# Performance work log

Measured on AMD Instinct MI355X. Metric: run time of the kernel, lower is better.

## Reference

```python
import jax, jax.numpy as jnp
import numpy as np

N = 100000
E = 1600000
NEG_SLOPE = 0.2

def _gat_layer(x, src, dst, W, a_s, a_d, b, n):
    # GATConv (heads=1): h = xW; alpha_ij = softmax_i(leaky_relu(a_s.h_j + a_d.h_i))
    h = x @ W                                   # [N, F]
    s_src = h @ a_s                             # [N]
    s_dst = h @ a_d                             # [N]
    logits = jax.nn.leaky_relu(s_src[src] + s_dst[dst], NEG_SLOPE)  # [E]
    m = jax.ops.segment_max(logits, dst, num_segments=n)
    m = jnp.where(jnp.isfinite(m), m, 0.0)
    w = jnp.exp(logits - m[dst])
    denom = jax.ops.segment_sum(w, dst, num_segments=n)
    alpha = w / (denom[dst] + 1e-16)            # neighbor softmax per target node
    out = jax.ops.segment_sum(alpha[:, None] * h[src], dst, num_segments=n)
    return out + b

def setup_inputs() -> dict:
    key = jax.random.key(0)
    ks = jax.random.split(key, 12)
    def glorot(k, shape):
        fan = shape[0] + shape[-1] if len(shape) > 1 else shape[0]
        return jax.random.normal(k, shape, jnp.float32) * jnp.sqrt(2.0 / fan)
    x = jax.random.normal(ks[0], (N, 128), jnp.float32)
    edge_index = jax.random.randint(ks[1], (2, E), 0, N, dtype=jnp.int32)
    return {
        'x': x, 'edge_index': edge_index,
        'W1': glorot(ks[2], (128, 64)), 'a1s': glorot(ks[3], (64,)), 'a1d': glorot(ks[4], (64,)), 'b1': jnp.zeros((64,), jnp.float32),
        'W2': glorot(ks[5], (64, 64)), 'a2s': glorot(ks[6], (64,)), 'a2d': glorot(ks[7], (64,)), 'b2': jnp.zeros((64,), jnp.float32),
        'W3': glorot(ks[8], (64, 32)), 'a3s': glorot(ks[9], (32,)), 'a3d': glorot(ks[10], (32,)), 'b3': jnp.zeros((32,), jnp.float32),
    }

def reference(x, edge_index, W1, a1s, a1d, b1, W2, a2s, a2d, b2, W3, a3s, a3d, b3):
    n = x.shape[0]
    # PyG GATConv adds self-loops by default
    loops = jnp.arange(n, dtype=edge_index.dtype)
    src = jnp.concatenate([edge_index[0], loops])
    dst = jnp.concatenate([edge_index[1], loops])
    h = _gat_layer(x, src, dst, W1, a1s, a1d, b1, n)
    h = jax.nn.relu(h)  # dropout is identity in eval mode
    h = _gat_layer(h, src, dst, W2, a2s, a2d, b2, n)
    h = jax.nn.relu(h)
    h = _gat_layer(h, src, dst, W3, a3s, a3d, b3, n)
    return jax.nn.log_softmax(h, axis=1)
```

## Files before the change

kernel.cpp:

```cpp
#include <hip/hip_runtime.h>
#include <hip/hip_fp16.h>
#include <cstddef>
#include <cstdint>

#define NEG_SLOPE 0.2f

__device__ __forceinline__ unsigned short f2bf(float f) {
    unsigned int u = __float_as_uint(f);
    u = (u + 0x7fff + ((u >> 16) & 1)) >> 16;
    return (unsigned short)u;
}
__device__ __forceinline__ float bf_lo(unsigned int u) { return __uint_as_float(u << 16); }
__device__ __forceinline__ float bf_hi(unsigned int u) { return __uint_as_float(u & 0xffff0000u); }

typedef __attribute__((ext_vector_type(8))) short bf16x8;
typedef __attribute__((ext_vector_type(4))) float f32x4;
typedef __attribute__((ext_vector_type(2))) float f32x2;


constexpr int BIN_BLOCKS = 256;
constexpr int MAX_NBK = 1024;

__global__ __launch_bounds__(256) void zero_k(int* __restrict__ p, int n) {
    int i = blockIdx.x * blockDim.x + threadIdx.x;
    if (i < n) p[i] = 0;
}

__global__ __launch_bounds__(256) void bin_hist_k(const int* __restrict__ dst, int E,
                                                  int* __restrict__ btot,
                                                  int* __restrict__ blkoff,
                                                  int nbk, int chunk) {
    __shared__ int hist[MAX_NBK];
    for (int i = threadIdx.x; i < nbk; i += 256) hist[i] = 0;
    __syncthreads();
    const int lo = blockIdx.x * chunk;
    const int hi = min(lo + chunk, E);
    for (int e = lo + threadIdx.x; e < hi; e += 256)
        atomicAdd(&hist[dst[e] >> 7], 1);
    __syncthreads();
    const int B = gridDim.x;
    for (int i = threadIdx.x; i < nbk; i += 256)
        blkoff[i * B + blockIdx.x] = atomicAdd(&btot[i], hist[i]);
}

__global__ __launch_bounds__(256) void scan_small_k(const int* __restrict__ btot,
                                                    int* __restrict__ obk, int nbk) {
    __shared__ int sh[MAX_NBK];
    const int tid = threadIdx.x;
    for (int i = tid; i < nbk; i += 256) sh[i] = btot[i];
    __syncthreads();
    if (tid == 0) {
        int run = 0;
        for (int i = 0; i < nbk; ++i) { int c = sh[i]; sh[i] = run; run += c; }
        obk[nbk] = run;
    }
    __syncthreads();
    for (int i = tid; i < nbk; i += 256) obk[i] = sh[i];
}

__global__ __launch_bounds__(256) void bin_scatter_k(const int* __restrict__ ei, int E,
                                                     const int* __restrict__ obk,
                                                     const int* __restrict__ blkoff,
                                                     int* __restrict__ eb, int nbk,
                                                     int chunk) {
    __shared__ int cur[MAX_NBK];
    __shared__ int off_s[MAX_NBK];
    const int B = gridDim.x;
    for (int i = threadIdx.x; i < nbk; i += 256) {
        cur[i] = 0;
        off_s[i] = obk[i] + blkoff[i * B + blockIdx.x];
    }
    __syncthreads();
    const int lo = blockIdx.x * chunk;
    const int hi = min(lo + chunk, E);
    for (int e = lo + threadIdx.x; e < hi; e += 256) {
        int s = ei[e];
        int d = ei[E + e];
        int b = d >> 7;
        int idx = atomicAdd(&cur[b], 1);
        eb[off_s[b] + idx] = (s << 7) | (d & 127);
    }
}

__global__ __launch_bounds__(256) void bucket_build_k(const int* __restrict__ eb,
                                                      const int* __restrict__ obk,
                                                      int* __restrict__ row_ptr,
                                                      int* __restrict__ col,
                                                      int n, int nbk) {
    __shared__ int c[128];
    __shared__ int rp[128];
    const int b = blockIdx.x;
    const int t = threadIdx.x;
    const int beg = obk[b];
    const int end = obk[b + 1];
    const int bbase = beg + b * 128;
    if (t < 128) c[t] = 1;
    __syncthreads();
    for (int i = beg + t; i < end; i += 256)
        atomicAdd(&c[eb[i] & 127], 1);
    __syncthreads();
    if (t < 64) {
        int v0 = c[2 * t], v1 = c[2 * t + 1];
        int pair = v0 + v1;
        int inc = pair;
        for (int o = 1; o < 64; o <<= 1) {
            int u = __shfl_up(inc, o);
            if (t >= o) inc += u;
        }
        int ex = inc - pair;
        rp[2 * t] = bbase + ex;
        rp[2 * t + 1] = bbase + ex + v0;
    }
    __syncthreads();
    const int node = b * 128 + t;
    if (t < 128 && node < n) {
        row_ptr[node] = rp[t];
        col[rp[t]] = node;
    }
    if (b == 0 && t == 0) row_ptr[n] = obk[nbk] + n;
    __syncthreads();
    if (t < 128) c[t] = 1;
    __syncthreads();
    for (int i = beg + t; i < end; i += 256) {
        int p = eb[i];
        int dl = p & 127;
        int idx = atomicAdd(&c[dl], 1);
        col[rp[dl] + idx] = p >> 7;
    }
}


template <int K, int F, bool BIN>
__launch_bounds__(256)
__global__ void gemm_mfma_k(const void* __restrict__ xin, const float* __restrict__ W,
                            const float* __restrict__ a_s, const float* __restrict__ a_d,
                            unsigned short* __restrict__ hb, float* __restrict__ ss,
                            float* __restrict__ sd, int n) {
    constexpr int MT = 64;
    constexpr int KP = K + 8;
    constexpr int NT = F / 16;
    constexpr int KC = K / 32;

    __shared__ unsigned short xb[MT * KP];
    __shared__ unsigned short wb[F * KP];

    const int tid = threadIdx.x;
    const int lane = tid & 63;
    const int wv = tid >> 6;
    const int base = blockIdx.x * MT;

    if (BIN) {
        const unsigned short* x = (const unsigned short*)xin;
        for (int i = tid; i < MT * K / 8; i += 256) {
            int row = i / (K / 8);
            int c8 = i % (K / 8);
            uint4 v = make_uint4(0u, 0u, 0u, 0u);
            if (base + row < n)
                v = *(const uint4*)&x[(size_t)(base + row) * K + 8 * c8];
            *(uint4*)&xb[row * KP + 8 * c8] = v;
        }
    } else {
        const float* x = (const float*)xin;
        for (int i = tid; i < MT * K / 4; i += 256) {
            int row = i / (K / 4);
            int c4 = i % (K / 4);
            float4 v = make_float4(0.f, 0.f, 0.f, 0.f);
            if (base + row < n)
                v = *(const float4*)&x[(size_t)(base + row) * K + 4 * c4];
            ushort4 b;
            b.x = f2bf(v.x); b.y = f2bf(v.y); b.z = f2bf(v.z); b.w = f2bf(v.w);
            *(ushort4*)&xb[row * KP + 4 * c4] = b;
        }
    }
    for (int i = tid; i < K * F / 4; i += 256) {
        int k = i / (F / 4);
        int n4 = i % (F / 4);
        float4 v = *(const float4*)&W[(size_t)k * F + 4 * n4];
        wb[(4 * n4 + 0) * KP + k] = f2bf(v.x);
        wb[(4 * n4 + 1) * KP + k] = f2bf(v.y);
        wb[(4 * n4 + 2) * KP + k] = f2bf(v.z);
        wb[(4 * n4 + 3) * KP + k] = f2bf(v.w);
    }
    __syncthreads();

    const int mrow = lane & 15;
    const int quad = lane >> 4;

    f32x4 acc[NT];
#pragma unroll
    for (int t = 0; t < NT; ++t) acc[t] = (f32x4){0.f, 0.f, 0.f, 0.f};

#pragma unroll
    for (int kc = 0; kc < KC; ++kc) {
        const int kof = kc * 32 + quad * 8;
        bf16x8 af = *(const bf16x8*)&xb[(wv * 16 + mrow) * KP + kof];
#pragma unroll
        for (int t = 0; t < NT; ++t) {
            bf16x8 bf = *(const bf16x8*)&wb[(t * 16 + mrow) * KP + kof];
            acc[t] = __builtin_amdgcn_mfma_f32_16x16x32_bf16(af, bf, acc[t], 0, 0, 0);
        }
    }

    float as_c[NT], ad_c[NT];
#pragma unroll
    for (int t = 0; t < NT; ++t) { as_c[t] = a_s[t * 16 + mrow]; ad_c[t] = a_d[t * 16 + mrow]; }

#pragma unroll
    for (int r = 0; r < 4; ++r) {
        const int node = base + wv * 16 + quad * 4 + r;
        float ps = 0.f, pd = 0.f;
#pragma unroll
        for (int t = 0; t < NT; ++t) {
            ps = fmaf(acc[t][r], as_c[t], ps);
            pd = fmaf(acc[t][r], ad_c[t], pd);
        }
#pragma unroll
        for (int o = 1; o < 16; o <<= 1) {
            ps += __shfl_xor(ps, o);
            pd += __shfl_xor(pd, o);
        }
        if (node < n) {
#pragma unroll
            for (int t = 0; t < NT; ++t)
                hb[(size_t)node * F + t * 16 + mrow] = f2bf(acc[t][r]);
            if (mrow == 0) { ss[node] = ps; sd[node] = pd; }
        }
    }
}


template <int F, int S, bool RELU, bool LOGSM, bool OUTB>
__launch_bounds__(256)
__global__ void gat_agg_k(const int* __restrict__ row_ptr, const int* __restrict__ col,
                          const unsigned short* __restrict__ hb,
                          const float* __restrict__ ss, const float* __restrict__ sd,
                          const float* __restrict__ bias,
                          void* __restrict__ outv, int n) {
    constexpr int NPW = 64 / S;
    constexpr int NL = F / 8;
    constexpr int Q = S / NL;
    const int lane = threadIdx.x & 63;
    const int ls   = lane % S;
    const int q    = ls / NL;
    const int cl   = ls % NL;
    const int lbase = lane - ls;
    const int wave = (blockIdx.x * blockDim.x + threadIdx.x) >> 6;
    const int node = wave * NPW + lane / S;
    if (node >= n) return;

    const int beg = row_ptr[node];
    const int end = row_ptr[node + 1];
    const float sdv = sd[node];
    float z0 = ss[node] + sdv;
    z0 = (z0 > 0.f) ? z0 : NEG_SLOPE * z0;

    float s = 0.f;
    f32x2 acc2[4];
#pragma unroll
    for (int i = 0; i < 4; ++i) acc2[i] = (f32x2){0.f, 0.f};

    for (int base = beg; base < end; base += S) {
        const int j = base + ls;
        int   c = 0;
        float logit = -__builtin_inff();
        if (j < end) {
            c = col[j];
            float z = ss[c] + sdv;
            logit = (z > 0.f) ? z : NEG_SLOPE * z;
        }
        const float w = __expf(logit - z0);
        s += w;
        const unsigned int pk = ((unsigned int)f2bf(w) << 17) | (unsigned int)c;

        auto gather = [&](int tt) {
            const unsigned int pe = __shfl(pk, lbase + Q * tt + q);
            const int ct = (int)(pe & 0x1ffffu);
            const float wt = __uint_as_float((pe >> 17) << 16);
            const uint4 hv = *(const uint4*)&hb[(size_t)ct * F + 8 * cl];
            f32x2 p;
            p.x = bf_lo(hv.x); p.y = bf_hi(hv.x); acc2[0] += p * wt;
            p.x = bf_lo(hv.y); p.y = bf_hi(hv.y); acc2[1] += p * wt;
            p.x = bf_lo(hv.z); p.y = bf_hi(hv.z); acc2[2] += p * wt;
            p.x = bf_lo(hv.w); p.y = bf_hi(hv.w); acc2[3] += p * wt;
        };

        const int cnt = min(S, end - base);
        int t = 0;
        for (; Q * (t + 3) < cnt; t += 4) {
            gather(t); gather(t + 1); gather(t + 2); gather(t + 3);
        }
        for (; Q * (t + 1) < cnt; t += 2) { gather(t); gather(t + 1); }
        if (Q * t < cnt) gather(t);
    }

#pragma unroll
    for (int o = S / 2; o; o >>= 1) s += __shfl_xor(s, o);
    float val[8] = {acc2[0].x, acc2[0].y, acc2[1].x, acc2[1].y,
                    acc2[2].x, acc2[2].y, acc2[3].x, acc2[3].y};
#pragma unroll
    for (int o = NL; o < S; o <<= 1) {
#pragma unroll
        for (int i = 0; i < 8; ++i) val[i] += __shfl_xor(val[i], o);
    }

    const float inv = 1.f / (s + 1e-16f);
#pragma unroll
    for (int i = 0; i < 8; ++i) {
        val[i] = val[i] * inv + bias[8 * cl + i];
        if (RELU) val[i] = fmaxf(val[i], 0.f);
    }
    if (LOGSM) {
        float lm = val[0];
#pragma unroll
        for (int i = 1; i < 8; ++i) lm = fmaxf(lm, val[i]);
#pragma unroll
        for (int o = 1; o < NL; o <<= 1) lm = fmaxf(lm, __shfl_xor(lm, o));
        float ex = 0.f;
#pragma unroll
        for (int i = 0; i < 8; ++i) ex += __expf(val[i] - lm);
#pragma unroll
        for (int o = 1; o < NL; o <<= 1) ex += __shfl_xor(ex, o);
        const float lse = lm + __logf(ex);
#pragma unroll
        for (int i = 0; i < 8; ++i) val[i] -= lse;
    }
    if (q == 0) {
        if (OUTB) {
            unsigned short* out = (unsigned short*)outv;
            ushort4 p0, p1;
            p0.x = f2bf(val[0]); p0.y = f2bf(val[1]); p0.z = f2bf(val[2]); p0.w = f2bf(val[3]);
            p1.x = f2bf(val[4]); p1.y = f2bf(val[5]); p1.z = f2bf(val[6]); p1.w = f2bf(val[7]);
            *(ushort4*)&out[(size_t)node * F + 8 * cl] = p0;
            *(ushort4*)&out[(size_t)node * F + 8 * cl + 4] = p1;
        } else {
            float* out = (float*)outv;
            float4 v0 = make_float4(val[0], val[1], val[2], val[3]);
            float4 v1 = make_float4(val[4], val[5], val[6], val[7]);
            *(float4*)&out[(size_t)node * F + 8 * cl] = v0;
            *(float4*)&out[(size_t)node * F + 8 * cl + 4] = v1;
        }
    }
}


extern "C" void kernel_launch(void* const* d_in, const int* in_sizes, int n_in,
                              void* d_out, int out_size, void* d_ws, size_t ws_size,
                              hipStream_t stream) {
    const float* x  = (const float*)d_in[0];
    const int*   ei = (const int*)d_in[1];
    const float* W1 = (const float*)d_in[2];
    const float* a1s = (const float*)d_in[3];
    const float* a1d = (const float*)d_in[4];
    const float* b1  = (const float*)d_in[5];
    const float* W2 = (const float*)d_in[6];
    const float* a2s = (const float*)d_in[7];
    const float* a2d = (const float*)d_in[8];
    const float* b2  = (const float*)d_in[9];
    const float* W3 = (const float*)d_in[10];
    const float* a3s = (const float*)d_in[11];
    const float* a3d = (const float*)d_in[12];
    const float* b3  = (const float*)d_in[13];

    const int N = in_sizes[0] / 128;
    const int E = in_sizes[1] / 2;
    const int NBK = (N + 127) / 128;
    const int B = BIN_BLOCKS;

    char* wp = (char*)d_ws;
    auto alloc = [&](size_t bytes) -> void* {
        void* p = wp;
        wp += (bytes + 255) & ~(size_t)255;
        return p;
    };
    int* row_ptr = (int*)alloc((size_t)(N + 1) * 4);
    int* col     = (int*)alloc((size_t)(E + N) * 4);
    unsigned short* hb  = (unsigned short*)alloc((size_t)N * 64 * 2);
    float* ss  = (float*)alloc((size_t)N * 4);
    float* sd  = (float*)alloc((size_t)N * 4);
    unsigned short* o1b = (unsigned short*)alloc((size_t)N * 64 * 2);
    unsigned short* o2b = (unsigned short*)alloc((size_t)N * 64 * 2);
    int* btot   = (int*)alloc((size_t)NBK * 4);
    int* blkoff = (int*)alloc((size_t)NBK * B * 4);
    int* obk    = (int*)alloc((size_t)(NBK + 1) * 4);
    int* eb     = (int*)alloc((size_t)E * 4);

    const int chunk = (E + B - 1) / B;

    zero_k<<<(NBK + 255) / 256, 256, 0, stream>>>(btot, NBK);
    bin_hist_k<<<B, 256, 0, stream>>>(ei + E, E, btot, blkoff, NBK, chunk);
    scan_small_k<<<1, 256, 0, stream>>>(btot, obk, NBK);
    bin_scatter_k<<<B, 256, 0, stream>>>(ei, E, obk, blkoff, eb, NBK, chunk);
    bucket_build_k<<<NBK, 256, 0, stream>>>(eb, obk, row_ptr, col, N, NBK);

    const int GB = (N + 63) / 64;

    gemm_mfma_k<128, 64, false><<<GB, 256, 0, stream>>>(x, W1, a1s, a1d, hb, ss, sd, N);
    gat_agg_k<64, 32, true, false, true><<<(N + 7) / 8, 256, 0, stream>>>(
        row_ptr, col, hb, ss, sd, b1, o1b, N);

    gemm_mfma_k<64, 64, true><<<GB, 256, 0, stream>>>(o1b, W2, a2s, a2d, hb, ss, sd, N);
    gat_agg_k<64, 32, true, false, true><<<(N + 7) / 8, 256, 0, stream>>>(
        row_ptr, col, hb, ss, sd, b2, o2b, N);

    gemm_mfma_k<64, 32, true><<<GB, 256, 0, stream>>>(o2b, W3, a3s, a3d, hb, ss, sd, N);
    gat_agg_k<32, 16, false, true, false><<<(N + 15) / 16, 256, 0, stream>>>(
        row_ptr, col, hb, ss, sd, b3, d_out, N);
}
```

Baseline: 309.0 us.

## Fuse GAT aggregation with next layer's GEMM and parallelize bucket scan

Adds agg_gemm_k, which runs the neighbour-softmax aggregation of layers 1 and 2 into a shared-memory tile and then feeds it straight into the next layer's bf16 MFMA GEMM and attention-score dot products. This drops the round trip of the intermediate activations through global memory and removes two kernel launches. Each layer now gets its own h/ss/sd buffers, and the single-thread prefix scan becomes a wavefront shuffle scan. The aggregation replaces the running max with a self-loop logit shift and packs bf16 weights next to 17-bit column indices, which caps node ids at 131072. Half of the 512 threads sit idle during the GEMM phase.

```diff
diff --git a/kernel.cpp b/kernel.cpp
--- a/kernel.cpp
+++ b/kernel.cpp
@@ -1,5 +1,4 @@
 #include <hip/hip_runtime.h>
-#include <hip/hip_fp16.h>
 #include <cstddef>
 #include <cstdint>
 
@@ -49,10 +48,21 @@
     const int tid = threadIdx.x;
     for (int i = tid; i < nbk; i += 256) sh[i] = btot[i];
     __syncthreads();
-    if (tid == 0) {
+    if (tid < 64) {
         int run = 0;
-        for (int i = 0; i < nbk; ++i) { int c = sh[i]; sh[i] = run; run += c; }
-        obk[nbk] = run;
+        for (int b0 = 0; b0 < nbk; b0 += 64) {
+            const int i = b0 + tid;
+            int v = (i < nbk) ? sh[i] : 0;
+            int inc = v;
+#pragma unroll
+            for (int o = 1; o < 64; o <<= 1) {
+                int u = __shfl_up(inc, o);
+                if (tid >= o) inc += u;
+            }
+            if (i < nbk) sh[i] = run + inc - v;
+            run += __shfl(inc, 63);
+        }
+        if (tid == 0) obk[nbk] = run;
     }
     __syncthreads();
     for (int i = tid; i < nbk; i += 256) obk[i] = sh[i];
@@ -130,9 +140,9 @@
 }
 
 
-template <int K, int F, bool BIN>
+template <int K, int F>
 __launch_bounds__(256)
-__global__ void gemm_mfma_k(const void* __restrict__ xin, const float* __restrict__ W,
+__global__ void gemm_mfma_k(const float* __restrict__ x, const float* __restrict__ W,
                             const float* __restrict__ a_s, const float* __restrict__ a_d,
                             unsigned short* __restrict__ hb, float* __restrict__ ss,
                             float* __restrict__ sd, int n) {
@@ -149,37 +159,25 @@
     const int wv = tid >> 6;
     const int base = blockIdx.x * MT;
 
-    if (BIN) {
-        const unsigned short* x = (const unsigned short*)xin;
-        for (int i = tid; i < MT * K / 8; i += 256) {
-            int row = i / (K / 8);
-            int c8 = i % (K / 8);
-            uint4 v = make_uint4(0u, 0u, 0u, 0u);
-            if (base + row < n)
-                v = *(const uint4*)&x[(size_t)(base + row) * K + 8 * c8];
-            *(uint4*)&xb[row * KP + 8 * c8] = v;
-        }
-    } else {
-        const float* x = (const float*)xin;
-        for (int i = tid; i < MT * K / 4; i += 256) {
-            int row = i / (K / 4);
-            int c4 = i % (K / 4);
-            float4 v = make_float4(0.f, 0.f, 0.f, 0.f);
-            if (base + row < n)
-                v = *(const float4*)&x[(size_t)(base + row) * K + 4 * c4];
-            ushort4 b;
-            b.x = f2bf(v.x); b.y = f2bf(v.y); b.z = f2bf(v.z); b.w = f2bf(v.w);
-            *(ushort4*)&xb[row * KP + 4 * c4] = b;
-        }
+    for (int i = tid; i < MT * K / 4; i += 256) {
+        int row = i / (K / 4);
+        int c4 = i % (K / 4);
+        float4 v = make_float4(0.f, 0.f, 0.f, 0.f);
+        if (base + row < n)
+            v = *(const float4*)&x[(size_t)(base + row) * K + 4 * c4];
+        ushort4 b;
+        b.x = f2bf(v.x); b.y = f2bf(v.y); b.z = f2bf(v.z); b.w = f2bf(v.w);
+        *(ushort4*)&xb[row * KP + 4 * c4] = b;
     }
     for (int i = tid; i < K * F / 4; i += 256) {
-        int k = i / (F / 4);
-        int n4 = i % (F / 4);
-        float4 v = *(const float4*)&W[(size_t)k * F + 4 * n4];
-        wb[(4 * n4 + 0) * KP + k] = f2bf(v.x);
-        wb[(4 * n4 + 1) * KP + k] = f2bf(v.y);
-        wb[(4 * n4 + 2) * KP + k] = f2bf(v.z);
-        wb[(4 * n4 + 3) * KP + k] = f2bf(v.w);
+        int nn = i % F;
+        int k4 = i / F;
+        ushort4 b;
+        b.x = f2bf(W[(size_t)(4 * k4 + 0) * F + nn]);
+        b.y = f2bf(W[(size_t)(4 * k4 + 1) * F + nn]);
+        b.z = f2bf(W[(size_t)(4 * k4 + 2) * F + nn]);
+        b.w = f2bf(W[(size_t)(4 * k4 + 3) * F + nn]);
+        *(ushort4*)&wb[nn * KP + 4 * k4] = b;
     }
     __syncthreads();
 
@@ -196,8 +194,8 @@
         bf16x8 af = *(const bf16x8*)&xb[(wv * 16 + mrow) * KP + kof];
 #pragma unroll
         for (int t = 0; t < NT; ++t) {
-            bf16x8 bf = *(const bf16x8*)&wb[(t * 16 + mrow) * KP + kof];
-            acc[t] = __builtin_amdgcn_mfma_f32_16x16x32_bf16(af, bf, acc[t], 0, 0, 0);
+            bf16x8 bfr = *(const bf16x8*)&wb[(t * 16 + mrow) * KP + kof];
+            acc[t] = __builtin_amdgcn_mfma_f32_16x16x32_bf16(af, bfr, acc[t], 0, 0, 0);
         }
     }
 
@@ -224,6 +222,159 @@
             for (int t = 0; t < NT; ++t)
                 hb[(size_t)node * F + t * 16 + mrow] = f2bf(acc[t][r]);
             if (mrow == 0) { ss[node] = ps; sd[node] = pd; }
+        }
+    }
+}
+
+
+template <int K, int F>
+__launch_bounds__(512)
+__global__ void agg_gemm_k(const int* __restrict__ row_ptr, const int* __restrict__ col,
+                           const unsigned short* __restrict__ hbi,
+                           const float* __restrict__ ssi, const float* __restrict__ sdi,
+                           const float* __restrict__ bias,
+                           const float* __restrict__ W,
+                           const float* __restrict__ a_s, const float* __restrict__ a_d,
+                           unsigned short* __restrict__ hbo, float* __restrict__ sso,
+                           float* __restrict__ sdo, int n) {
+    static_assert(K == 64, "agg phase assumes 64 input channels");
+    constexpr int S = 8;
+    constexpr int MT = 64;
+    constexpr int KP = K + 8;
+    constexpr int NT = F / 16;
+    constexpr int KC = K / 32;
+
+    __shared__ unsigned short xb[MT * KP];
+    __shared__ unsigned short wb[F * KP];
+
+    const int tid = threadIdx.x;
+    const int lane = tid & 63;
+    const int wv = tid >> 6;
+    const int base = blockIdx.x * MT;
+
+    for (int i = tid; i < K * F / 4; i += 512) {
+        int nn = i % F;
+        int k4 = i / F;
+        ushort4 b;
+        b.x = f2bf(W[(size_t)(4 * k4 + 0) * F + nn]);
+        b.y = f2bf(W[(size_t)(4 * k4 + 1) * F + nn]);
+        b.z = f2bf(W[(size_t)(4 * k4 + 2) * F + nn]);
+        b.w = f2bf(W[(size_t)(4 * k4 + 3) * F + nn]);
+        *(ushort4*)&wb[nn * KP + 4 * k4] = b;
+    }
+
+    const int ls = lane & (S - 1);
+    const int lbase = lane - ls;
+    const int nl = tid >> 3;
+    const int node = base + nl;
+
+    float val[8] = {0.f, 0.f, 0.f, 0.f, 0.f, 0.f, 0.f, 0.f};
+    if (node < n) {
+        const int beg = row_ptr[node];
+        const int end = row_ptr[node + 1];
+        const float sdv = sdi[node];
+        float z0 = ssi[node] + sdv;
+        z0 = (z0 > 0.f) ? z0 : NEG_SLOPE * z0;
+
+        float s = 0.f;
+        f32x2 acc2[4];
+#pragma unroll
+        for (int i = 0; i < 4; ++i) acc2[i] = (f32x2){0.f, 0.f};
+
+        for (int b0 = beg; b0 < end; b0 += S) {
+            const int j = b0 + ls;
+            int   c = 0;
+            float logit = -__builtin_inff();
+            if (j < end) {
+                c = col[j];
+                float z = ssi[c] + sdv;
+                logit = (z > 0.f) ? z : NEG_SLOPE * z;
+            }
+            const float w = __expf(logit - z0);
+            s += w;
+            const unsigned int pk = ((unsigned int)f2bf(w) << 17) | (unsigned int)c;
+
+            auto gather = [&](int tt) {
+                const unsigned int pe = __shfl(pk, lbase + tt);
+                const int ct = (int)(pe & 0x1ffffu);
+                const float wt = __uint_as_float((pe >> 17) << 16);
+                const uint4 hv = *(const uint4*)&hbi[(size_t)ct * K + 8 * ls];
+                f32x2 p;
+                p.x = bf_lo(hv.x); p.y = bf_hi(hv.x); acc2[0] += p * wt;
+                p.x = bf_lo(hv.y); p.y = bf_hi(hv.y); acc2[1] += p * wt;
+                p.x = bf_lo(hv.z); p.y = bf_hi(hv.z); acc2[2] += p * wt;
+                p.x = bf_lo(hv.w); p.y = bf_hi(hv.w); acc2[3] += p * wt;
+            };
+
+            const int cnt = min(S, end - b0);
+            int t = 0;
+            for (; t + 3 < cnt; t += 4) {
+                gather(t); gather(t + 1); gather(t + 2); gather(t + 3);
+            }
+            for (; t < cnt; ++t) gather(t);
+        }
+#pragma unroll
+        for (int o = S / 2; o; o >>= 1) s += __shfl_xor(s, o);
+        const float inv = 1.f / (s + 1e-16f);
+        val[0] = acc2[0].x; val[1] = acc2[0].y; val[2] = acc2[1].x; val[3] = acc2[1].y;
+        val[4] = acc2[2].x; val[5] = acc2[2].y; val[6] = acc2[3].x; val[7] = acc2[3].y;
+#pragma unroll
+        for (int i = 0; i < 8; ++i)
+            val[i] = fmaxf(val[i] * inv + bias[8 * ls + i], 0.f);
+    }
+    {
+        ushort4 p0, p1;
+        p0.x = f2bf(val[0]); p0.y = f2bf(val[1]); p0.z = f2bf(val[2]); p0.w = f2bf(val[3]);
+        p1.x = f2bf(val[4]); p1.y = f2bf(val[5]); p1.z = f2bf(val[6]); p1.w = f2bf(val[7]);
+        *(ushort4*)&xb[nl * KP + 8 * ls] = p0;
+        *(ushort4*)&xb[nl * KP + 8 * ls + 4] = p1;
+    }
+
+    __syncthreads();
+
+    if (wv < 4) {
+        const int mrow = lane & 15;
+        const int quad = lane >> 4;
+
+        f32x4 acc[NT];
+#pragma unroll
+        for (int t = 0; t < NT; ++t) acc[t] = (f32x4){0.f, 0.f, 0.f, 0.f};
+
+#pragma unroll
+        for (int kc = 0; kc < KC; ++kc) {
+            const int kof = kc * 32 + quad * 8;
+            bf16x8 af = *(const bf16x8*)&xb[(wv * 16 + mrow) * KP + kof];
+#pragma unroll
+            for (int t = 0; t < NT; ++t) {
+                bf16x8 bfr = *(const bf16x8*)&wb[(t * 16 + mrow) * KP + kof];
+                acc[t] = __builtin_amdgcn_mfma_f32_16x16x32_bf16(af, bfr, acc[t], 0, 0, 0);
+            }
+        }
+
+        float as_c[NT], ad_c[NT];
+#pragma unroll
+        for (int t = 0; t < NT; ++t) { as_c[t] = a_s[t * 16 + mrow]; ad_c[t] = a_d[t * 16 + mrow]; }
+
+#pragma unroll
+        for (int r = 0; r < 4; ++r) {
+            const int node2 = base + wv * 16 + quad * 4 + r;
+            float ps = 0.f, pd = 0.f;
+#pragma unroll
+            for (int t = 0; t < NT; ++t) {
+                ps = fmaf(acc[t][r], as_c[t], ps);
+                pd = fmaf(acc[t][r], ad_c[t], pd);
+            }
+#pragma unroll
+            for (int o = 1; o < 16; o <<= 1) {
+                ps += __shfl_xor(ps, o);
+                pd += __shfl_xor(pd, o);
+            }
+            if (node2 < n) {
+#pragma unroll
+                for (int t = 0; t < NT; ++t)
+                    hbo[(size_t)node2 * F + t * 16 + mrow] = f2bf(acc[t][r]);
+                if (mrow == 0) { sso[node2] = ps; sdo[node2] = pd; }
+            }
         }
     }
 }
@@ -374,11 +525,15 @@
     };
     int* row_ptr = (int*)alloc((size_t)(N + 1) * 4);
     int* col     = (int*)alloc((size_t)(E + N) * 4);
-    unsigned short* hb  = (unsigned short*)alloc((size_t)N * 64 * 2);
-    float* ss  = (float*)alloc((size_t)N * 4);
-    float* sd  = (float*)alloc((size_t)N * 4);
-    unsigned short* o1b = (unsigned short*)alloc((size_t)N * 64 * 2);
-    unsigned short* o2b = (unsigned short*)alloc((size_t)N * 64 * 2);
+    unsigned short* hb1 = (unsigned short*)alloc((size_t)N * 64 * 2);
+    unsigned short* hb2 = (unsigned short*)alloc((size_t)N * 64 * 2);
+    unsigned short* hb3 = (unsigned short*)alloc((size_t)N * 32 * 2);
+    float* ss1 = (float*)alloc((size_t)N * 4);
+    float* sd1 = (float*)alloc((size_t)N * 4);
+    float* ss2 = (float*)alloc((size_t)N * 4);
+    float* sd2 = (float*)alloc((size_t)N * 4);
+    float* ss3 = (float*)alloc((size_t)N * 4);
+    float* sd3 = (float*)alloc((size_t)N * 4);
     int* btot   = (int*)alloc((size_t)NBK * 4);
     int* blkoff = (int*)alloc((size_t)NBK * B * 4);
     int* obk    = (int*)alloc((size_t)(NBK + 1) * 4);
@@ -394,15 +549,11 @@
 
     const int GB = (N + 63) / 64;
 
-    gemm_mfma_k<128, 64, false><<<GB, 256, 0, stream>>>(x, W1, a1s, a1d, hb, ss, sd, N);
-    gat_agg_k<64, 32, true, false, true><<<(N + 7) / 8, 256, 0, stream>>>(
-        row_ptr, col, hb, ss, sd, b1, o1b, N);
-
-    gemm_mfma_k<64, 64, true><<<GB, 256, 0, stream>>>(o1b, W2, a2s, a2d, hb, ss, sd, N);
-    gat_agg_k<64, 32, true, false, true><<<(N + 7) / 8, 256, 0, stream>>>(
-        row_ptr, col, hb, ss, sd, b2, o2b, N);
-
-    gemm_mfma_k<64, 32, true><<<GB, 256, 0, stream>>>(o2b, W3, a3s, a3d, hb, ss, sd, N);
+    gemm_mfma_k<128, 64><<<GB, 256, 0, stream>>>(x, W1, a1s, a1d, hb1, ss1, sd1, N);
+    agg_gemm_k<64, 64><<<GB, 512, 0, stream>>>(row_ptr, col, hb1, ss1, sd1, b1,
+                                               W2, a2s, a2d, hb2, ss2, sd2, N);
+    agg_gemm_k<64, 32><<<GB, 512, 0, stream>>>(row_ptr, col, hb2, ss2, sd2, b2,
+                                               W3, a3s, a3d, hb3, ss3, sd3, N);
     gat_agg_k<32, 16, false, true, false><<<(N + 15) / 16, 256, 0, stream>>>(
-        row_ptr, col, hb, ss, sd, b3, d_out, N);
-}
+        row_ptr, col, hb3, ss3, sd3, b3, d_out, N);
+}
```

New measurement: 288.6 us. -6.6%, faster.
